# Performance work log

Hardware: AMD Instinct MI355X
Metric: run time of the kernel (lower is better)

## Reference

```python
import jax, jax.numpy as jnp
import numpy as np

B, Q, K, D, H = 8, 128, 1024, 256, 256


def setup_inputs() -> dict:
    key = jax.random.key(0)
    ks = jax.random.split(key, 7)
    queries = jax.random.normal(ks[0], (B, Q, D), dtype=jnp.float32)
    keys = jax.random.normal(ks[1], (B, K, D), dtype=jnp.float32)
    values = jax.random.normal(ks[2], (B, K, D), dtype=jnp.float32)
    W_q = jax.random.normal(ks[3], (H, D), dtype=jnp.float32) * (1.0 / np.sqrt(D))
    W_k = jax.random.normal(ks[4], (H, D), dtype=jnp.float32) * (1.0 / np.sqrt(D))
    w_v = jax.random.normal(ks[5], (H,), dtype=jnp.float32) * (1.0 / np.sqrt(H))
    valid_lens = jax.random.randint(ks[6], (B,), 0, K, dtype=jnp.int64)
    return {"queries": queries, "keys": keys, "values": values,
            "W_q": W_q, "W_k": W_k, "w_v": w_v, "valid_lens": valid_lens}


def reference(queries, keys, values, W_q, W_k, w_v, valid_lens):
    # Linear projections (bias=False): [B,Q,H], [B,K,H]
    q = jnp.einsum("bqd,hd->bqh", queries, W_q)
    k = jnp.einsum("bkd,hd->bkh", keys, W_k)
    # Broadcast add -> tanh -> reduce with w_v: scores [B,Q,K]
    features = jnp.tanh(q[:, :, None, :] + k[:, None, :, :])  # [B,Q,K,H]
    scores = jnp.einsum("bqkh,h->bqk", features, w_v)
    # Masked softmax over K: positions >= valid_len get -1e9
    mask = jnp.arange(K)[None, None, :] < valid_lens[:, None, None]
    scores = jnp.where(mask, scores, jnp.float32(-1e9))
    attn = jax.nn.softmax(scores, axis=-1)  # [B,Q,K]
    # Dropout p=0.0 (eval): identity. bmm(attn, values) -> [B,Q,Dv]
    return jnp.einsum("bqk,bkv->bqv", attn, values)
```

## Files before the change

### kernel.cpp

```cpp
#include <hip/hip_runtime.h>

#define BB 8
#define QQ 128
#define KK 1024
#define DD 256
#define HH 256

#define KSP 32
#define KCH 32

#define TWO_LOG2E     2.8853900817779268f
#define NEG_TWO_LOG2E -2.8853900817779268f

__global__ __launch_bounds__(256) void proj_kernel(const float* __restrict__ queries,
                                                   const float* __restrict__ keys,
                                                   const float* __restrict__ Wq,
                                                   const float* __restrict__ Wk,
                                                   const int* __restrict__ vlen,
                                                   float* __restrict__ eproj) {
    const int r0 = blockIdx.x * 64;
    const bool isQ = (r0 < BB * QQ);
    if (!isQ) {
        const int kb = (r0 - BB * QQ) >> 6;
        const int b  = kb >> 4;
        const int k0 = (kb & 15) << 6;
        if (k0 >= vlen[b]) return;
    }

    __shared__ float As[64][68];
    __shared__ float Ws[64][68];
    const int t  = threadIdx.x;
    const int tr = t & 15;
    const int th = t >> 4;
    const int h0 = blockIdx.y * 64;
    const float* A = isQ ? (queries + (size_t)r0 * DD)
                         : (keys + (size_t)(r0 - BB * QQ) * DD);
    const float* W = isQ ? Wq : Wk;

    float acc[4][4] = {};

    for (int dc = 0; dc < DD; dc += 64) {
#pragma unroll
        for (int i = 0; i < 4; ++i) {
            int fi  = t + 256 * i;
            int row = fi >> 4;
            int c4  = (fi & 15) << 2;
            *(float4*)&As[row][c4] = *(const float4*)&A[(size_t)row * DD + dc + c4];
            *(float4*)&Ws[row][c4] = *(const float4*)&W[(size_t)(h0 + row) * DD + dc + c4];
        }
        __syncthreads();
#pragma unroll 4
        for (int dd = 0; dd < 64; dd += 4) {
            float4 a4[4], w4[4];
#pragma unroll
            for (int i = 0; i < 4; ++i) a4[i] = *(float4*)&As[tr + 16 * i][dd];
#pragma unroll
            for (int i = 0; i < 4; ++i) w4[i] = *(float4*)&Ws[th + 16 * i][dd];
#pragma unroll
            for (int ri = 0; ri < 4; ++ri)
#pragma unroll
                for (int hi = 0; hi < 4; ++hi) {
                    acc[ri][hi] += a4[ri].x * w4[hi].x + a4[ri].y * w4[hi].y +
                                   a4[ri].z * w4[hi].z + a4[ri].w * w4[hi].w;
                }
        }
        __syncthreads();
    }
#pragma unroll
    for (int ri = 0; ri < 4; ++ri)
#pragma unroll
        for (int hi = 0; hi < 4; ++hi) {
            eproj[(size_t)(r0 + tr + 16 * ri) * HH + h0 + th + 16 * hi] =
                __builtin_amdgcn_exp2f(TWO_LOG2E * acc[ri][hi]);
        }
}

__global__ __launch_bounds__(512, 4) void scoreav_kernel(const float* __restrict__ eproj,
                                                         const float* __restrict__ wv,
                                                         const int* __restrict__ vlen,
                                                         const float* __restrict__ V,
                                                         float* __restrict__ partial,
                                                         float* __restrict__ psum) {
    int id = blockIdx.x;
    int b = 0;
    bool found = false;
#pragma unroll
    for (int bb = 0; bb < BB; ++bb) {
        if (!found) {
            int v = vlen[bb];
            int cnt = ((v == 0) ? KSP : ((v + KCH - 1) / KCH)) * 4;
            if (id < cnt) { b = bb; found = true; }
            else id -= cnt;
        }
    }
    if (!found) return;
    const int ksb = id >> 2;
    const int q0  = (id & 3) * 32;
    const int k0  = ksb * KCH;
    const int vl  = vlen[b];

    __shared__ float st[2][32][260];
    __shared__ float pT[KCH][36];
    float* red = &st[0][0][0];

    const int t = threadIdx.x;
    const int w = t >> 6;
    const int l = t & 63;
    const int ql = l & 7;
    const int kl = l >> 3;

    float acc[4][4] = {};

    if (vl > 0) {
#pragma unroll
        for (int i = 0; i < 8; ++i) {
            int fi  = t + 512 * i;
            int row = fi >> 6;
            int c4  = (fi & 63) << 2;
            size_t gr = (row < 32) ? (size_t)(b * QQ + q0 + row)
                                   : (size_t)(BB * QQ + b * KK + k0 + row - 32);
            *(float4*)&st[row >> 5][row & 31][c4] =
                *(const float4*)&eproj[gr * HH + c4];
        }
        __syncthreads();

        const int hw = 32 * w;
#pragma unroll
        for (int hh = 0; hh < 32; hh += 4) {
            const float4 w4 = *(const float4*)&wv[hw + hh];
            const float* wa = (const float*)&w4;
            float4 q4[4], k4[4];
#pragma unroll
            for (int i = 0; i < 4; ++i) q4[i] = *(float4*)&st[0][ql + 8 * i][hw + hh];
#pragma unroll
            for (int j = 0; j < 4; ++j) k4[j] = *(float4*)&st[1][kl + 8 * j][hw + hh];
#pragma unroll
            for (int i = 0; i < 4; ++i) {
                const float* qa = (const float*)&q4[i];
#pragma unroll
                for (int j = 0; j < 4; ++j) {
                    const float* ka = (const float*)&k4[j];
#pragma unroll
                    for (int c = 0; c < 4; ++c) {
                        float d = __builtin_fmaf(qa[c], ka[c], 1.0f);
                        acc[i][j] += wa[c] * __builtin_amdgcn_rcpf(d);
                    }
                }
            }
        }
        __syncthreads();

#pragma unroll
        for (int i = 0; i < 4; ++i)
#pragma unroll
            for (int j = 0; j < 4; ++j)
                red[w * 1056 + (ql + 8 * i) * 33 + (kl + 8 * j)] = acc[i][j];
    }
    __syncthreads();

    float pvv[2];
#pragma unroll
    for (int u = 0; u < 2; ++u) {
        int n = t + 512 * u;
        int q = n >> 5, k = n & 31;
        float s = 0.f;
        if (vl > 0) {
#pragma unroll
            for (int ww = 0; ww < 8; ++ww) s += red[ww * 1056 + q * 33 + k];
        }
        int kg = k0 + k;
        float pv;
        if (vl == 0) pv = 1.0f;
        else pv = (kg < vl) ? __builtin_amdgcn_exp2f(NEG_TWO_LOG2E * s) : 0.0f;
        pT[k][q] = pv;
        pvv[u] = pv;
    }
    float s0 = pvv[0], s1 = pvv[1];
#pragma unroll
    for (int off = 1; off < 32; off <<= 1) {
        s0 += __shfl_xor(s0, off);
        s1 += __shfl_xor(s1, off);
    }
    if ((l & 31) == 0) {
        int qa = 2 * w + (l >> 5);
        psum[((size_t)ksb * BB + b) * QQ + q0 + qa]      = s0;
        psum[((size_t)ksb * BB + b) * QQ + q0 + qa + 16] = s1;
    }
    __syncthreads();

    const float* VB = V + ((size_t)b * KK + k0) * DD;
    const int d4 = (t & 63) << 2;
    const int qg = w << 2;
    float4 a4[4] = {};
#pragma unroll 4
    for (int k = 0; k < KCH; ++k) {
        float4 v4 = *(const float4*)&VB[(size_t)k * DD + d4];
        float4 p4 = *(float4*)&pT[k][qg];
        a4[0].x += p4.x * v4.x; a4[0].y += p4.x * v4.y; a4[0].z += p4.x * v4.z; a4[0].w += p4.x * v4.w;
        a4[1].x += p4.y * v4.x; a4[1].y += p4.y * v4.y; a4[1].z += p4.y * v4.z; a4[1].w += p4.y * v4.w;
        a4[2].x += p4.z * v4.x; a4[2].y += p4.z * v4.y; a4[2].z += p4.z * v4.z; a4[2].w += p4.z * v4.w;
        a4[3].x += p4.w * v4.x; a4[3].y += p4.w * v4.y; a4[3].z += p4.w * v4.z; a4[3].w += p4.w * v4.w;
    }
#pragma unroll
    for (int qi = 0; qi < 4; ++qi) {
        int q = q0 + qg + qi;
        *(float4*)&partial[(((size_t)ksb * BB + b) * QQ + q) * DD + d4] = a4[qi];
    }
}

__global__ __launch_bounds__(256) void av_reduce(const float* __restrict__ partial,
                                                 const float* __restrict__ psum,
                                                 const int* __restrict__ vlen,
                                                 float* __restrict__ out) {
    const int i  = blockIdx.x * 256 + threadIdx.x;
    const int bq = i >> 6;
    const int b  = bq >> 7;
    const int vl = vlen[b];
    const int nch = (vl == 0) ? KSP : ((vl + KCH - 1) / KCH);

    float S = 0.f;
    for (int ks = 0; ks < nch; ++ks) S += psum[(size_t)ks * (BB * QQ) + bq];

    const float4* p4 = (const float4*)partial;
    const int stride4 = BB * QQ * DD / 4;
    float4 s = {0.f, 0.f, 0.f, 0.f};
    for (int ks = 0; ks < nch; ++ks) {
        float4 x = p4[(size_t)ks * stride4 + i];
        s.x += x.x; s.y += x.y; s.z += x.z; s.w += x.w;
    }
    const float inv = 1.0f / S;
    s.x *= inv; s.y *= inv; s.z *= inv; s.w *= inv;
    ((float4*)out)[i] = s;
}

extern "C" void kernel_launch(void* const* d_in, const int* in_sizes, int n_in,
                              void* d_out, int out_size, void* d_ws, size_t ws_size,
                              hipStream_t stream) {
    const float* queries = (const float*)d_in[0];
    const float* keys    = (const float*)d_in[1];
    const float* values  = (const float*)d_in[2];
    const float* W_q     = (const float*)d_in[3];
    const float* W_k     = (const float*)d_in[4];
    const float* w_v     = (const float*)d_in[5];
    const int*   vlen    = (const int*)d_in[6];
    float* out = (float*)d_out;

    float* ws      = (float*)d_ws;
    float* eproj   = ws;
    float* psum    = eproj + (size_t)(BB * QQ + BB * KK) * HH;
    float* partial = psum + (size_t)KSP * BB * QQ;

    proj_kernel<<<dim3((BB * QQ + BB * KK) / 64, HH / 64, 1), 256, 0, stream>>>(
        queries, keys, W_q, W_k, vlen, eproj);

    scoreav_kernel<<<dim3(KSP * 4 * BB, 1, 1), 512, 0, stream>>>(
        eproj, w_v, vlen, values, partial, psum);

    av_reduce<<<dim3(BB * QQ * DD / 4 / 256, 1, 1), 256, 0, stream>>>(
        partial, psum, vlen, out);
}
```

Before: 143.1 us.

## Split projection reduction over D into two partial slices, combine in score kernel

The projection kernel now splits the D=256 reduction into two halves via a third grid dimension. Each half writes a scaled partial sum to its own buffer. The score kernel loads both partials, adds them and applies exp2 when staging into shared memory. The aim is to double the block count of the projection kernel for better occupancy, at the cost of twice the workspace writes and an extra global read in the consumer.

```diff
diff --git a/kernel.cpp b/kernel.cpp
--- a/kernel.cpp
+++ b/kernel.cpp
@@ -9,6 +9,9 @@
 #define KSP 32
 #define KCH 32
 
+#define RTOT (BB * QQ + BB * KK)
+#define PSTRIDE ((size_t)RTOT * HH)
+
 #define TWO_LOG2E     2.8853900817779268f
 #define NEG_TWO_LOG2E -2.8853900817779268f
 
@@ -17,7 +20,7 @@
                                                    const float* __restrict__ Wq,
                                                    const float* __restrict__ Wk,
                                                    const int* __restrict__ vlen,
-                                                   float* __restrict__ eproj) {
+                                                   float* __restrict__ pp) {
     const int r0 = blockIdx.x * 64;
     const bool isQ = (r0 < BB * QQ);
     if (!isQ) {
@@ -33,13 +36,14 @@
     const int tr = t & 15;
     const int th = t >> 4;
     const int h0 = blockIdx.y * 64;
+    const int dc0 = blockIdx.z * 128;
     const float* A = isQ ? (queries + (size_t)r0 * DD)
                          : (keys + (size_t)(r0 - BB * QQ) * DD);
     const float* W = isQ ? Wq : Wk;
 
     float acc[4][4] = {};
 
-    for (int dc = 0; dc < DD; dc += 64) {
+    for (int dc = dc0; dc < dc0 + 128; dc += 64) {
 #pragma unroll
         for (int i = 0; i < 4; ++i) {
             int fi  = t + 256 * i;
@@ -66,16 +70,18 @@
         }
         __syncthreads();
     }
+
+    float* outp = pp + (size_t)blockIdx.z * PSTRIDE;
 #pragma unroll
     for (int ri = 0; ri < 4; ++ri)
 #pragma unroll
         for (int hi = 0; hi < 4; ++hi) {
-            eproj[(size_t)(r0 + tr + 16 * ri) * HH + h0 + th + 16 * hi] =
-                __builtin_amdgcn_exp2f(TWO_LOG2E * acc[ri][hi]);
-        }
-}
-
-__global__ __launch_bounds__(512, 4) void scoreav_kernel(const float* __restrict__ eproj,
+            outp[(size_t)(r0 + tr + 16 * ri) * HH + h0 + th + 16 * hi] =
+                TWO_LOG2E * acc[ri][hi];
+        }
+}
+
+__global__ __launch_bounds__(512, 4) void scoreav_kernel(const float* __restrict__ pp,
                                                          const float* __restrict__ wv,
                                                          const int* __restrict__ vlen,
                                                          const float* __restrict__ V,
@@ -119,8 +125,15 @@
             int c4  = (fi & 63) << 2;
             size_t gr = (row < 32) ? (size_t)(b * QQ + q0 + row)
                                    : (size_t)(BB * QQ + b * KK + k0 + row - 32);
-            *(float4*)&st[row >> 5][row & 31][c4] =
-                *(const float4*)&eproj[gr * HH + c4];
+            const float* base = pp + gr * HH + c4;
+            float4 v0 = *(const float4*)base;
+            float4 v1 = *(const float4*)(base + PSTRIDE);
+            float4 s;
+            s.x = __builtin_amdgcn_exp2f(v0.x + v1.x);
+            s.y = __builtin_amdgcn_exp2f(v0.y + v1.y);
+            s.z = __builtin_amdgcn_exp2f(v0.z + v1.z);
+            s.w = __builtin_amdgcn_exp2f(v0.w + v1.w);
+            *(float4*)&st[row >> 5][row & 31][c4] = s;
         }
         __syncthreads();
 
@@ -246,15 +259,15 @@
     float* out = (float*)d_out;
 
     float* ws      = (float*)d_ws;
-    float* eproj   = ws;
-    float* psum    = eproj + (size_t)(BB * QQ + BB * KK) * HH;
+    float* pp      = ws;
+    float* psum    = pp + 2 * PSTRIDE;
     float* partial = psum + (size_t)KSP * BB * QQ;
 
-    proj_kernel<<<dim3((BB * QQ + BB * KK) / 64, HH / 64, 1), 256, 0, stream>>>(
-        queries, keys, W_q, W_k, vlen, eproj);
+    proj_kernel<<<dim3(RTOT / 64, HH / 64, 2), 256, 0, stream>>>(
+        queries, keys, W_q, W_k, vlen, pp);
 
     scoreav_kernel<<<dim3(KSP * 4 * BB, 1, 1), 512, 0, stream>>>(
-        eproj, w_v, vlen, values, partial, psum);
+        pp, w_v, vlen, values, partial, psum);
 
     av_reduce<<<dim3(BB * QQ * DD / 4 / 256, 1, 1), 256, 0, stream>>>(
         partial, psum, vlen, out);
```

After: 142.5 us (median of 2 runs). No clear change (-0.4%).
